# Kernel tuning notes

Hardware: AMD Instinct MI355X
Metric: run time of the kernel (lower is better)

Reference implementation:

```python
import jax, jax.numpy as jnp
import numpy as np

CHEB_K = 3
ORDER = 2


def setup_inputs() -> dict:
    key = jax.random.key(0)
    ks = jax.random.split(key, 7)
    B, C, N, T = 16, 64, 2048, 12
    E, O = 10, 64
    x = jax.random.normal(ks[0], (B, C, N, T), jnp.float32)
    node_embeddings = jax.random.normal(ks[1], (N, E), jnp.float32)
    # nonnegative row-normalized adjacency for the diffusion branch
    a = jax.random.uniform(ks[2], (1, N, N), jnp.float32)
    support = a / jnp.sum(a, axis=-1, keepdims=True)
    weights_pool = 0.05 * jax.random.normal(ks[3], (E, CHEB_K, C, O), jnp.float32)
    bias_pool = 0.05 * jax.random.normal(ks[4], (E, O), jnp.float32)
    mlp_w = 0.05 * jax.random.normal(ks[5], ((ORDER * 1 + 1) * C, O), jnp.float32)
    mlp_b = 0.05 * jax.random.normal(ks[6], (O,), jnp.float32)
    return {
        "x": x,
        "node_embeddings": node_embeddings,
        "support": support,
        "weights_pool": weights_pool,
        "bias_pool": bias_pool,
        "mlp_w": mlp_w,
        "mlp_b": mlp_b,
    }


def reference(x, node_embeddings, support, weights_pool, bias_pool, mlp_w, mlp_b):
    # ---- adaptive Chebyshev branch ----
    N = node_embeddings.shape[0]
    A = jax.nn.softmax(jax.nn.relu(node_embeddings @ node_embeddings.T), axis=1)  # [N,N]
    supports = [jnp.eye(N, dtype=A.dtype), A]
    for _ in range(2, CHEB_K):
        supports.append(2.0 * (A @ supports[-1]) - supports[-2])
    S = jnp.stack(supports, axis=0)                         # [K,N,N]
    weights = jnp.einsum('nd,dkio->nkio', node_embeddings, weights_pool)  # [N,K,C,O]
    bias = node_embeddings @ bias_pool                      # [N,O]
    # x: [B,C,N,T]; diffuse then contract per-node weights
    x_g = jnp.einsum('knm,bimw->bwnki', S, x)               # [B,T,N,K,C]
    x_av = jnp.einsum('bwnki,nkio->bwno', x_g, weights) + bias  # [B,T,N,O]
    x_av = x_av.transpose(0, 3, 2, 1)                       # [B,O,N,T]

    # ---- diffusion conv branch ----
    out = [x]
    for si in range(support.shape[0]):
        a = support[si]                                     # [N,N]
        x1 = jnp.einsum('bcvl,vw->bcwl', x, a)
        out.append(x1)
        for _ in range(2, ORDER + 1):
            x1 = jnp.einsum('bcvl,vw->bcwl', x1, a)
            out.append(x1)
    xg = jnp.concatenate(out, axis=1)                       # [B,(order*S+1)*C,N,T]
    # 1x1 Conv2d == channel matmul; dropout is identity in eval mode
    x_gcn = jnp.einsum('bcnw,co->bonw', xg, mlp_w) + mlp_b[None, :, None, None]
    return x_av, x_gcn
```

## Files before the change

kernel.cpp:

```cpp
#include <hip/hip_runtime.h>
#include <stdint.h>

#define NN    2048
#define BB    16
#define CC    64
#define TT    12
#define OO    64
#define ED    10
#define JJ    12288
#define NJ    25165824
#define KC    192

typedef __attribute__((ext_vector_type(8))) short short8;
typedef __attribute__((ext_vector_type(4))) float f32x4;

__device__ __forceinline__ unsigned short f2bf(float x) {
    union { float f; unsigned int u; } v; v.f = x;
    unsigned int r = (v.u + 0x7FFFu + ((v.u >> 16) & 1u)) >> 16;
    return (unsigned short)r;
}
__device__ __forceinline__ float bf2f(unsigned short h) {
    union { unsigned int u; float f; } v; v.u = ((unsigned int)h) << 16;
    return v.f;
}
__device__ __forceinline__ void async_cp16(const void* g, void* l) {
    __builtin_amdgcn_global_load_lds(
        (const __attribute__((address_space(1))) void*)(uintptr_t)g,
        (__attribute__((address_space(3))) void*)(uintptr_t)l, 16, 0, 0);
}

__global__ __launch_bounds__(256) void k_softmax_A(const float* __restrict__ E,
                                                   unsigned short* __restrict__ Abf) {
    int n = blockIdx.x, tid = threadIdx.x;
    __shared__ float row[NN];
    __shared__ float red[256];
    float en[ED];
#pragma unroll
    for (int d = 0; d < ED; ++d) en[d] = E[n * ED + d];
    float mx = 0.0f;
    for (int m = tid; m < NN; m += 256) {
        float s = 0.f;
#pragma unroll
        for (int d = 0; d < ED; ++d) s += en[d] * E[m * ED + d];
        s = fmaxf(s, 0.0f);
        row[m] = s;
        mx = fmaxf(mx, s);
    }
    red[tid] = mx; __syncthreads();
    for (int s = 128; s; s >>= 1) { if (tid < s) red[tid] = fmaxf(red[tid], red[tid + s]); __syncthreads(); }
    mx = red[0]; __syncthreads();
    float sum = 0.f;
    for (int m = tid; m < NN; m += 256) { float e = __expf(row[m] - mx); row[m] = e; sum += e; }
    red[tid] = sum; __syncthreads();
    for (int s = 128; s; s >>= 1) { if (tid < s) red[tid] += red[tid + s]; __syncthreads(); }
    float inv = 1.0f / red[0];
    for (int m = tid; m < NN; m += 256) Abf[(size_t)n * NN + m] = f2bf(row[m] * inv);
}

__global__ void k_trans_bf(const float* __restrict__ src, unsigned short* __restrict__ dst) {
    __shared__ float t[32][33];
    int tx = threadIdx.x, ty = threadIdx.y;
    int x0 = blockIdx.x * 32, y0 = blockIdx.y * 32;
#pragma unroll
    for (int i = 0; i < 4; ++i)
        t[ty + i * 8][tx] = src[(size_t)(y0 + ty + i * 8) * NN + x0 + tx];
    __syncthreads();
#pragma unroll
    for (int i = 0; i < 4; ++i)
        dst[(size_t)(x0 + ty + i * 8) * NN + y0 + tx] = f2bf(t[tx][ty + i * 8]);
}

__global__ __launch_bounds__(256) void k_make_X2(const float* __restrict__ x,
                                                 unsigned short* __restrict__ X2) {
    int idx = blockIdx.x * 256 + threadIdx.x;
    int n = idx / JJ;
    int r = idx - n * JJ;
    int bt = r >> 6;
    int c = r & 63;
    int b = bt / TT;
    int t = bt - b * TT;
    X2[idx] = f2bf(x[(((size_t)b * CC + c) * NN + n) * TT + t]);
}

__global__ __launch_bounds__(256) void k_trans16(const unsigned short* __restrict__ src,
                                                 unsigned short* __restrict__ dst) {
    __shared__ unsigned short t[64][72];
    int tid = threadIdx.x;
    int j0 = blockIdx.x * 64, n0 = blockIdx.y * 64;
    int r = tid >> 3, c8 = (tid & 7) * 8;
#pragma unroll
    for (int it = 0; it < 2; ++it) {
        int rr = r + it * 32;
        *(short8*)&t[rr][c8] = *(const short8*)&src[(size_t)(n0 + rr) * JJ + j0 + c8];
    }
    __syncthreads();
#pragma unroll
    for (int it = 0; it < 2; ++it) {
        int rr = r + it * 32;
        unsigned short v[8];
#pragma unroll
        for (int u = 0; u < 8; ++u) v[u] = t[c8 + u][rr];
        *(short8*)&dst[(size_t)(j0 + rr) * NN + n0 + c8] = *(short8*)v;
    }
}

__global__ __launch_bounds__(256) void k_gemm(const unsigned short* __restrict__ Am,
                                              const unsigned short* __restrict__ Bt,
                                              unsigned short* __restrict__ Out,
                                              const unsigned short* __restrict__ Csub,
                                              float alpha) {
    __shared__ __align__(16) unsigned short lA[128 * 32];
    __shared__ __align__(16) unsigned short lB[128 * 32];
    int tid = threadIdx.x, lane = tid & 63, wv = tid >> 6;
    int m0 = blockIdx.y * 128, j0 = blockIdx.x * 128;
    int wm = (wv >> 1) * 64, wn = (wv & 1) * 64;
    f32x4 zero = {0.f, 0.f, 0.f, 0.f};
    f32x4 acc[4][4];
#pragma unroll
    for (int a = 0; a < 4; ++a)
#pragma unroll
        for (int b = 0; b < 4; ++b) acc[a][b] = zero;

    int q = lane >> 4, l15 = lane & 15;
    int rA = lane >> 2;
    int cA = (lane & 3) * 8;

    const unsigned short* gA = Am + (size_t)(m0 + (lane >> 2)) * 2048 + cA;
    const unsigned short* gB = Bt + (size_t)(j0 + (lane >> 2)) * 2048 + cA;

    for (int kt = 0; kt < 64; ++kt) {
        int k0 = kt * 32;
        __syncthreads();
#pragma unroll
        for (int c = 0; c < 2; ++c) {
            int g = wv + 4 * c;
            async_cp16(gA + (size_t)g * 16 * 2048 + k0, &lA[g * 512 + lane * 8]);
            async_cp16(gB + (size_t)g * 16 * 2048 + k0, &lB[g * 512 + lane * 8]);
        }
        __syncthreads();
        short8 af[4], bfr[4];
#pragma unroll
        for (int tm = 0; tm < 4; ++tm)
            af[tm] = *(const short8*)&lA[(wm + tm * 16 + l15) * 32 + q * 8];
#pragma unroll
        for (int tn = 0; tn < 4; ++tn)
            bfr[tn] = *(const short8*)&lB[(wn + tn * 16 + l15) * 32 + q * 8];
#pragma unroll
        for (int tm = 0; tm < 4; ++tm)
#pragma unroll
            for (int tn = 0; tn < 4; ++tn)
                acc[tm][tn] = __builtin_amdgcn_mfma_f32_16x16x32_bf16(af[tm], bfr[tn], acc[tm][tn], 0, 0, 0);
    }
#pragma unroll
    for (int tm = 0; tm < 4; ++tm) {
#pragma unroll
        for (int tn = 0; tn < 4; ++tn) {
            int mm = m0 + wm + tm * 16 + q * 4;
            int jj = j0 + wn + tn * 16 + l15;
#pragma unroll
            for (int r = 0; r < 4; ++r) {
                size_t oidx = (size_t)(mm + r) * JJ + jj;
                float v = alpha * acc[tm][tn][r];
                if (Csub) v -= bf2f(Csub[oidx]);
                Out[oidx] = f2bf(v);
            }
        }
    }
}

__global__ __launch_bounds__(256) void k_node(const unsigned short* __restrict__ S0,
                                              const unsigned short* __restrict__ S1,
                                              const unsigned short* __restrict__ S2,
                                              const float* __restrict__ E,
                                              const float* __restrict__ Wp,
                                              const float* __restrict__ bias_pool,
                                              const float* __restrict__ mlp_w,
                                              const float* __restrict__ mlp_b,
                                              float* __restrict__ out,
                                              int branch) {
    int n = blockIdx.x, tid = threadIdx.x, lane = tid & 63, wv = tid >> 6;
    __shared__ __align__(16) unsigned short lW[64 * 200];
    __shared__ __align__(16) unsigned short lS[192 * 72];
    __shared__ float lBias[64];
    int q = lane >> 4, l15 = lane & 15;

    if (branch == 0) {
        float en[ED];
#pragma unroll
        for (int d = 0; d < ED; ++d) en[d] = E[n * ED + d];
        for (int idx = tid; idx < KC * OO; idx += 256) {
            int o = idx & 63, kap = idx >> 6;
            float s = 0.f;
#pragma unroll
            for (int d = 0; d < ED; ++d) s += en[d] * Wp[((size_t)d * KC + kap) * OO + o];
            lW[o * 200 + kap] = f2bf(s);
        }
        if (tid < 64) {
            float s = 0.f;
#pragma unroll
            for (int d = 0; d < ED; ++d) s += en[d] * bias_pool[d * OO + tid];
            lBias[tid] = s;
        }
    } else {
        for (int idx = tid; idx < KC * OO; idx += 256) {
            int o = idx & 63, kap = idx >> 6;
            lW[o * 200 + kap] = f2bf(mlp_w[kap * OO + o]);
        }
        if (tid < 64) lBias[tid] = mlp_b[tid];
    }

    f32x4 zero = {0.f, 0.f, 0.f, 0.f};
    f32x4 acc[3][4];
#pragma unroll
    for (int a = 0; a < 3; ++a)
#pragma unroll
        for (int b = 0; b < 4; ++b) acc[a][b] = zero;

    const unsigned short* Ss[3] = { S0 + (size_t)n * JJ, S1 + (size_t)n * JJ, S2 + (size_t)n * JJ };

    for (int s = 0; s < 3; ++s) {
        __syncthreads();
#pragma unroll
        for (int v = 0; v < 6; ++v) {
            int e8 = (v * 256 + tid) * 8;
            int m = e8 >> 6, i = e8 & 63;
            *(short8*)&lS[m * 72 + i] = *(const short8*)&Ss[s][e8];
        }
        __syncthreads();
#pragma unroll
        for (int h = 0; h < 2; ++h) {
            short8 af[3], bfr[4];
#pragma unroll
            for (int tm = 0; tm < 3; ++tm)
                af[tm] = *(const short8*)&lS[(wv * 48 + tm * 16 + l15) * 72 + h * 32 + q * 8];
#pragma unroll
            for (int tn = 0; tn < 4; ++tn)
                bfr[tn] = *(const short8*)&lW[(tn * 16 + l15) * 200 + s * 64 + h * 32 + q * 8];
#pragma unroll
            for (int tm = 0; tm < 3; ++tm)
#pragma unroll
                for (int tn = 0; tn < 4; ++tn)
                    acc[tm][tn] = __builtin_amdgcn_mfma_f32_16x16x32_bf16(af[tm], bfr[tn], acc[tm][tn], 0, 0, 0);
        }
    }
#pragma unroll
    for (int tm = 0; tm < 3; ++tm) {
#pragma unroll
        for (int tn = 0; tn < 4; ++tn) {
            int o = tn * 16 + l15;
#pragma unroll
            for (int r = 0; r < 4; ++r) {
                int m = wv * 48 + tm * 16 + q * 4 + r;
                int b = m / TT, t = m - b * TT;
                out[(((size_t)b * OO + o) * NN + n) * TT + t] = acc[tm][tn][r] + lBias[o];
            }
        }
    }
}

extern "C" void kernel_launch(void* const* d_in, const int* in_sizes, int n_in,
                              void* d_out, int out_size, void* d_ws, size_t ws_size,
                              hipStream_t stream) {
    const float* x         = (const float*)d_in[0];
    const float* node_emb  = (const float*)d_in[1];
    const float* support   = (const float*)d_in[2];
    const float* wpool     = (const float*)d_in[3];
    const float* bpool     = (const float*)d_in[4];
    const float* mlp_w     = (const float*)d_in[5];
    const float* mlp_b     = (const float*)d_in[6];
    float* out             = (float*)d_out;

    unsigned short* Abf = (unsigned short*)d_ws;
    unsigned short* Atb = Abf + (size_t)NN * NN;
    unsigned short* b1  = Atb + (size_t)NN * NN;
    unsigned short* b2  = b1 + (size_t)NJ;
    unsigned short* b3  = b2 + (size_t)NJ;
    unsigned short* b4  = b3 + (size_t)NJ;
    unsigned short* b5  = b4 + (size_t)NJ;

    dim3 gg(96, 16);
    dim3 gt(192, 32);

    k_softmax_A<<<NN, 256, 0, stream>>>(node_emb, Abf);
    k_trans_bf<<<dim3(64, 64), dim3(32, 8), 0, stream>>>(support, Atb);
    k_make_X2<<<NJ / 256, 256, 0, stream>>>(x, b2);
    k_trans16<<<gt, 256, 0, stream>>>(b2, b1);

    k_gemm<<<gg, 256, 0, stream>>>(Abf, b1, b4, nullptr, 1.0f);
    k_trans16<<<gt, 256, 0, stream>>>(b4, b3);
    k_gemm<<<gg, 256, 0, stream>>>(Abf, b3, b5, b2, 2.0f);
    k_node<<<NN, 256, 0, stream>>>(b2, b4, b5, node_emb, wpool, bpool, nullptr, nullptr,
                                   out, 0);

    k_gemm<<<gg, 256, 0, stream>>>(Atb, b1, b4, nullptr, 1.0f);
    k_trans16<<<gt, 256, 0, stream>>>(b4, b3);
    k_gemm<<<gg, 256, 0, stream>>>(Atb, b3, b5, nullptr, 1.0f);
    k_node<<<NN, 256, 0, stream>>>(b2, b4, b5, nullptr, nullptr, nullptr, mlp_w, mlp_b,
                                   out + (size_t)NJ, 1);
}
```

Before: 1.116 ms.

## Replace bf16 GEMM with 256x256 tile, 8-wave, double-buffered pipelined kernel

Replaces the 128x128 single-buffered GEMM with a 256x256-tile, 512-thread kernel. It uses 128 KB of dynamic LDS split into double buffers, a K step of 64, XOR-swizzled LDS layout, block-index swizzling for L2 locality, and an interleaved load/MFMA phase schedule with setprio and vmcnt waits. The goal is to hide global-load latency, cut the two full syncs per K step, and raise MFMA utilisation on the four large diffusion GEMMs. The cost is higher register and LDS pressure and fragile hand-ordered waitcnt logic.

```diff
diff --git a/kernel.cpp b/kernel.cpp
--- a/kernel.cpp
+++ b/kernel.cpp
@@ -10,6 +10,7 @@
 #define JJ    12288
 #define NJ    25165824
 #define KC    192
+#define NTK   32
 
 typedef __attribute__((ext_vector_type(8))) short short8;
 typedef __attribute__((ext_vector_type(4))) float f32x4;
@@ -27,6 +28,12 @@
     __builtin_amdgcn_global_load_lds(
         (const __attribute__((address_space(1))) void*)(uintptr_t)g,
         (__attribute__((address_space(3))) void*)(uintptr_t)l, 16, 0, 0);
+}
+
+__device__ __forceinline__ void phase_barrier() {
+    asm volatile("" ::: "memory");
+    __builtin_amdgcn_s_barrier();
+    __builtin_amdgcn_sched_barrier(0);
 }
 
 __global__ __launch_bounds__(256) void k_softmax_A(const float* __restrict__ E,
@@ -104,63 +111,152 @@
     }
 }
 
-__global__ __launch_bounds__(256) void k_gemm(const unsigned short* __restrict__ Am,
-                                              const unsigned short* __restrict__ Bt,
-                                              unsigned short* __restrict__ Out,
-                                              const unsigned short* __restrict__ Csub,
-                                              float alpha) {
-    __shared__ __align__(16) unsigned short lA[128 * 32];
-    __shared__ __align__(16) unsigned short lB[128 * 32];
+template <int AOFF, int BOFF>
+__device__ __forceinline__ void mfma_quad(f32x4 (&acc)[8][4],
+                                          const short8 (&A)[4][2],
+                                          const short8 (&B)[2][2]) {
+    __builtin_amdgcn_s_setprio(1);
+#pragma unroll
+    for (int tm = 0; tm < 4; ++tm)
+#pragma unroll
+        for (int tn = 0; tn < 2; ++tn)
+#pragma unroll
+            for (int h = 0; h < 2; ++h)
+                acc[AOFF + tm][BOFF + tn] = __builtin_amdgcn_mfma_f32_16x16x32_bf16(
+                    A[tm][h], B[tn][h], acc[AOFF + tm][BOFF + tn], 0, 0, 0);
+    __builtin_amdgcn_s_setprio(0);
+}
+
+__global__ __launch_bounds__(512, 2) void k_gemm8(const unsigned short* __restrict__ Am,
+                                                  const unsigned short* __restrict__ Bt,
+                                                  unsigned short* __restrict__ Out,
+                                                  const unsigned short* __restrict__ Csub,
+                                                  float alpha) {
+    extern __shared__ char ldsc[];
     int tid = threadIdx.x, lane = tid & 63, wv = tid >> 6;
-    int m0 = blockIdx.y * 128, j0 = blockIdx.x * 128;
-    int wm = (wv >> 1) * 64, wn = (wv & 1) * 64;
-    f32x4 zero = {0.f, 0.f, 0.f, 0.f};
-    f32x4 acc[4][4];
-#pragma unroll
-    for (int a = 0; a < 4; ++a)
-#pragma unroll
-        for (int b = 0; b < 4; ++b) acc[a][b] = zero;
-
     int q = lane >> 4, l15 = lane & 15;
-    int rA = lane >> 2;
-    int cA = (lane & 3) * 8;
-
-    const unsigned short* gA = Am + (size_t)(m0 + (lane >> 2)) * 2048 + cA;
-    const unsigned short* gB = Bt + (size_t)(j0 + (lane >> 2)) * 2048 + cA;
-
-    for (int kt = 0; kt < 64; ++kt) {
-        int k0 = kt * 32;
-        __syncthreads();
-#pragma unroll
-        for (int c = 0; c < 2; ++c) {
-            int g = wv + 4 * c;
-            async_cp16(gA + (size_t)g * 16 * 2048 + k0, &lA[g * 512 + lane * 8]);
-            async_cp16(gB + (size_t)g * 16 * 2048 + k0, &lB[g * 512 + lane * 8]);
-        }
-        __syncthreads();
-        short8 af[4], bfr[4];
-#pragma unroll
-        for (int tm = 0; tm < 4; ++tm)
-            af[tm] = *(const short8*)&lA[(wm + tm * 16 + l15) * 32 + q * 8];
-#pragma unroll
-        for (int tn = 0; tn < 4; ++tn)
-            bfr[tn] = *(const short8*)&lB[(wn + tn * 16 + l15) * 32 + q * 8];
-#pragma unroll
-        for (int tm = 0; tm < 4; ++tm)
-#pragma unroll
-            for (int tn = 0; tn < 4; ++tn)
-                acc[tm][tn] = __builtin_amdgcn_mfma_f32_16x16x32_bf16(af[tm], bfr[tn], acc[tm][tn], 0, 0, 0);
-    }
-#pragma unroll
-    for (int tm = 0; tm < 4; ++tm) {
-#pragma unroll
-        for (int tn = 0; tn < 4; ++tn) {
-            int mm = m0 + wm + tm * 16 + q * 4;
-            int jj = j0 + wn + tn * 16 + l15;
+
+    int flat = blockIdx.y * 48 + blockIdx.x;
+    int swz = (flat & 7) * 48 + (flat >> 3);
+    int bx = swz % 48, by = swz / 48;
+    int j0g = bx * 256, m0g = by * 256;
+
+    int wmw = (wv >> 2) * 128;
+    int wnw = (wv & 3) * 64;
+
+    int srow = tid >> 3;
+    int scol = ((tid & 7) * 16) ^ ((srow & 7) << 4);
+    const char* srcA0 = (const char*)Am + (size_t)(m0g + srow) * 4096 + scol;
+    const char* srcB0 = (const char*)Bt + (size_t)(j0g + srow) * 4096 + scol;
+    char* dstA0 = ldsc + tid * 16;
+    char* dstB0 = ldsc + 32768 + tid * 16;
+
+#define STAGE_A(nb, kt, h)                                                                  \
+    do {                                                                                    \
+        async_cp16(srcA0 + (size_t)(kt) * 128 + (h) * 524288,                               \
+                   dstA0 + (nb) * 65536 + (h) * 16384);                                     \
+        async_cp16(srcA0 + (size_t)(kt) * 128 + (h) * 524288 + 262144,                      \
+                   dstA0 + (nb) * 65536 + (h) * 16384 + 8192);                              \
+    } while (0)
+#define STAGE_B(nb, kt, h)                                                                  \
+    do {                                                                                    \
+        async_cp16(srcB0 + (size_t)(kt) * 128 + (h) * 524288,                               \
+                   dstB0 + (nb) * 65536 + (h) * 16384);                                     \
+        async_cp16(srcB0 + (size_t)(kt) * 128 + (h) * 524288 + 262144,                      \
+                   dstB0 + (nb) * 65536 + (h) * 16384 + 8192);                              \
+    } while (0)
+
+    int rsw = (l15 & 7) << 4;
+    int colh0 = (q * 16) ^ rsw;
+    int colh1 = colh0 ^ 64;
+    int arA = (wmw + l15) * 128;
+    int arB = (wnw + l15) * 128;
+
+    f32x4 acc[8][4];
+#pragma unroll
+    for (int a = 0; a < 8; ++a)
+#pragma unroll
+        for (int b = 0; b < 4; ++b) acc[a][b] = (f32x4){0.f, 0.f, 0.f, 0.f};
+
+    STAGE_A(0, 0, 0);
+    STAGE_A(0, 0, 1);
+    STAGE_B(0, 0, 0);
+    STAGE_B(0, 0, 1);
+    STAGE_B(1, 1, 0);
+    STAGE_B(1, 1, 1);
+    asm volatile("s_waitcnt vmcnt(4)" ::: "memory");
+    __builtin_amdgcn_s_barrier();
+    __builtin_amdgcn_sched_barrier(0);
+
+    int cur = 0;
+    for (int t = 0; t < NTK; ++t, cur ^= 1) {
+        const int nb = cur ^ 1;
+        const char* pa = ldsc + (cur << 16);
+        const char* pA0 = pa + arA;
+        const char* pB0 = pa + 32768 + arB;
+
+        short8 af[4][2], bf0[2][2], bf1[2][2];
+
+#pragma unroll
+        for (int tm = 0; tm < 4; ++tm) {
+            af[tm][0] = *(const short8*)(pA0 + tm * 2048 + colh0);
+            af[tm][1] = *(const short8*)(pA0 + tm * 2048 + colh1);
+        }
+#pragma unroll
+        for (int tn = 0; tn < 2; ++tn) {
+            bf0[tn][0] = *(const short8*)(pB0 + tn * 2048 + colh0);
+            bf0[tn][1] = *(const short8*)(pB0 + tn * 2048 + colh1);
+        }
+        if (t + 1 < NTK) STAGE_A(nb, t + 1, 0);
+        phase_barrier();
+        mfma_quad<0, 0>(acc, af, bf0);
+        phase_barrier();
+
+#pragma unroll
+        for (int tn = 0; tn < 2; ++tn) {
+            bf1[tn][0] = *(const short8*)(pB0 + 4096 + tn * 2048 + colh0);
+            bf1[tn][1] = *(const short8*)(pB0 + 4096 + tn * 2048 + colh1);
+        }
+        if (t + 1 < NTK) STAGE_A(nb, t + 1, 1);
+        phase_barrier();
+        mfma_quad<0, 2>(acc, af, bf1);
+        phase_barrier();
+
+#pragma unroll
+        for (int tm = 0; tm < 4; ++tm) {
+            af[tm][0] = *(const short8*)(pA0 + 8192 + tm * 2048 + colh0);
+            af[tm][1] = *(const short8*)(pA0 + 8192 + tm * 2048 + colh1);
+        }
+        if (t + 2 < NTK) STAGE_B(cur, t + 2, 0);
+        phase_barrier();
+        mfma_quad<4, 2>(acc, af, bf1);
+        phase_barrier();
+
+        if (t + 2 < NTK) STAGE_B(cur, t + 2, 1);
+        phase_barrier();
+        mfma_quad<4, 0>(acc, af, bf0);
+        asm volatile("" ::: "memory");
+        if (t + 2 < NTK) {
+            asm volatile("s_waitcnt vmcnt(4)" ::: "memory");
+        } else if (t + 1 < NTK) {
+            asm volatile("s_waitcnt vmcnt(0)" ::: "memory");
+        }
+        __builtin_amdgcn_s_barrier();
+        __builtin_amdgcn_sched_barrier(0);
+    }
+#undef STAGE_A
+#undef STAGE_B
+
+#pragma unroll
+    for (int a = 0; a < 8; ++a) {
+        int mbase = m0g + wmw + (a >> 2) * 64 + (a & 3) * 16 + q * 4;
+#pragma unroll
+        for (int b = 0; b < 4; ++b) {
+            int jj = j0g + wnw + (b >> 1) * 32 + (b & 1) * 16 + l15;
 #pragma unroll
             for (int r = 0; r < 4; ++r) {
-                size_t oidx = (size_t)(mm + r) * JJ + jj;
-                float v = alpha * acc[tm][tn][r];
+                size_t oidx = (size_t)(mbase + r) * JJ + jj;
+                float v = alpha * acc[a][b][r];
                 if (Csub) v -= bf2f(Csub[oidx]);
                 Out[oidx] = f2bf(v);
             }
@@ -278,7 +374,14 @@
     unsigned short* b4  = b3 + (size_t)NJ;
     unsigned short* b5  = b4 + (size_t)NJ;
 
-    dim3 gg(96, 16);
+    static int attr_done = 0;
+    if (!attr_done) {
+        hipFuncSetAttribute(reinterpret_cast<const void*>(k_gemm8),
+                            hipFuncAttributeMaxDynamicSharedMemorySize, 131072);
+        attr_done = 1;
+    }
+
+    dim3 gg8(48, 8);
     dim3 gt(192, 32);
 
     k_softmax_A<<<NN, 256, 0, stream>>>(node_emb, Abf);
@@ -286,15 +389,15 @@
     k_make_X2<<<NJ / 256, 256, 0, stream>>>(x, b2);
     k_trans16<<<gt, 256, 0, stream>>>(b2, b1);
 
-    k_gemm<<<gg, 256, 0, stream>>>(Abf, b1, b4, nullptr, 1.0f);
+    k_gemm8<<<gg8, 512, 131072, stream>>>(Abf, b1, b4, nullptr, 1.0f);
     k_trans16<<<gt, 256, 0, stream>>>(b4, b3);
-    k_gemm<<<gg, 256, 0, stream>>>(Abf, b3, b5, b2, 2.0f);
+    k_gemm8<<<gg8, 512, 131072, stream>>>(Abf, b3, b5, b2, 2.0f);
     k_node<<<NN, 256, 0, stream>>>(b2, b4, b5, node_emb, wpool, bpool, nullptr, nullptr,
                                    out, 0);
 
-    k_gemm<<<gg, 256, 0, stream>>>(Atb, b1, b4, nullptr, 1.0f);
+    k_gemm8<<<gg8, 512, 131072, stream>>>(Atb, b1, b4, nullptr, 1.0f);
     k_trans16<<<gt, 256, 0, stream>>>(b4, b3);
-    k_gemm<<<gg, 256, 0, stream>>>(Atb, b3, b5, nullptr, 1.0f);
+    k_gemm8<<<gg8, 512, 131072, stream>>>(Atb, b3, b5, nullptr, 1.0f);
     k_node<<<NN, 256, 0, stream>>>(b2, b4, b5, nullptr, nullptr, nullptr, mlp_w, mlp_b,
                                    out + (size_t)NJ, 1);
 }
```

New measurement: 1.102 ms. Within noise of the previous version (-1.3%).
